# Kernel tuning notes

Hardware: AMD Instinct MI355X
Metric: run time of the kernel (lower is better)

Reference implementation:

```python
import jax, jax.numpy as jnp
import numpy as np

NUM_EMB = 512
LATENT = 20


def setup_inputs() -> dict:
    key = jax.random.key(0)
    ks = jax.random.split(key, 10)
    B = 262144
    c = jax.random.normal(ks[0], (B, 100), dtype=jnp.float32)
    W1 = jax.random.normal(ks[1], (100, 200), dtype=jnp.float32) * 0.1
    b1 = jnp.zeros((200,), dtype=jnp.float32)
    W2 = jax.random.normal(ks[2], (200, LATENT), dtype=jnp.float32) * 0.07
    b2 = jnp.zeros((LATENT,), dtype=jnp.float32)
    # codebook initialized uniform(-1/K, 1/K) as in torch
    codebook = jax.random.uniform(ks[3], (NUM_EMB, LATENT), dtype=jnp.float32,
                                  minval=-1.0 / NUM_EMB, maxval=1.0 / NUM_EMB)
    Wmu = jax.random.normal(ks[4], (LATENT, LATENT), dtype=jnp.float32) * 0.2
    bmu = jnp.zeros((LATENT,), dtype=jnp.float32)
    Wlv = jax.random.normal(ks[5], (LATENT, LATENT), dtype=jnp.float32) * 0.2
    blv = jnp.zeros((LATENT,), dtype=jnp.float32)
    return {"c": c, "W1": W1, "b1": b1, "W2": W2, "b2": b2,
            "codebook": codebook, "Wmu": Wmu, "bmu": bmu, "Wlv": Wlv, "blv": blv}


def reference(c, W1, b1, W2, b2, codebook, Wmu, bmu, Wlv, blv):
    # encoder: Linear -> ELU -> Linear
    h = jax.nn.elu(c @ W1 + b1)            # [B, 200]
    z_e = h @ W2 + b2                      # [B, 20]

    # vector quantization: pairwise squared distances to codebook
    d = (jnp.sum(z_e ** 2, axis=1, keepdims=True)
         + jnp.sum(codebook ** 2, axis=1)
         - 2.0 * z_e @ codebook.T)         # [B, K]
    idx = jnp.argmin(d, axis=1)            # [B]
    quantized = codebook[idx]              # [B, 20] gather

    commitment_loss = 0.25 * jnp.mean((jax.lax.stop_gradient(quantized) - z_e) ** 2)
    quantization_loss = jnp.mean((quantized - jax.lax.stop_gradient(z_e)) ** 2)
    z_q = z_e + jax.lax.stop_gradient(quantized - z_e)  # straight-through

    mu_c = z_e @ Wmu + bmu
    logvar_c = z_e @ Wlv + blv
    return (mu_c, logvar_c, z_q, z_e, quantization_loss, commitment_loss)
```

## Files before the change

### kernel.cpp

```cpp
#include <hip/hip_runtime.h>

typedef __bf16 bf16x8 __attribute__((ext_vector_type(8)));
typedef __bf16 bf16x4 __attribute__((ext_vector_type(4)));
typedef float  f32x4  __attribute__((ext_vector_type(4)));
typedef float  f32x2  __attribute__((ext_vector_type(2)));

constexpr int BN  = 262144;
constexpr int DIN = 100;
constexpr int DH  = 200;
constexpr int DZ  = 20;
constexpr int KCB = 512;

constexpr size_t WS_W1F  = 0;
constexpr size_t WS_W2F  = 53248;
constexpr size_t WS_CBF  = 69632;
constexpr size_t WS_WMUF = 102400;
constexpr size_t WS_WLVF = 104448;
constexpr size_t WS_B1P  = 106496;
constexpr size_t WS_B2P  = 107520;
constexpr size_t WS_BMUP = 107648;
constexpr size_t WS_BLVP = 107776;
constexpr size_t WS_PART = 107904;

constexpr int PN_W1 = 26624, PN_W2 = 8192, PN_CB = 16384, PN_WMU = 1024, PN_WLV = 1024;
constexpr int PN_TOT = PN_W1 + PN_W2 + PN_CB + PN_WMU + PN_WLV + 256 + 32 + 32 + 32;

__device__ __forceinline__ unsigned umin2(unsigned a, unsigned b) { return a < b ? a : b; }

__global__ __launch_bounds__(256) void prep_kernel(
    const float* __restrict__ W1, const float* __restrict__ b1,
    const float* __restrict__ W2, const float* __restrict__ b2,
    const float* __restrict__ cb,
    const float* __restrict__ Wmu, const float* __restrict__ bmu,
    const float* __restrict__ Wlv, const float* __restrict__ blv,
    unsigned char* __restrict__ ws)
{
    int e = blockIdx.x * 256 + threadIdx.x;
    if (e >= PN_TOT) return;
    __bf16* w1f  = (__bf16*)(ws + WS_W1F);
    __bf16* w2f  = (__bf16*)(ws + WS_W2F);
    __bf16* cbf  = (__bf16*)(ws + WS_CBF);
    __bf16* wmuf = (__bf16*)(ws + WS_WMUF);
    __bf16* wlvf = (__bf16*)(ws + WS_WLVF);
    float* b1p  = (float*)(ws + WS_B1P);
    float* b2p  = (float*)(ws + WS_B2P);
    float* bmup = (float*)(ws + WS_BMUP);
    float* blvp = (float*)(ws + WS_BLVP);

    if (e < PN_W1) {
        int j = e & 7, lane = (e >> 3) & 63, kk = (e >> 9) & 3, m = e >> 11;
        int n = m * 16 + (lane & 15);
        int k = kk * 32 + ((lane >> 4) << 3) + j;
        w1f[e] = (__bf16)((n < DH && k < DIN) ? W1[k * DH + n] : 0.f);
        return;
    }
    e -= PN_W1;
    if (e < PN_W2) {
        int j = e & 7, lane = (e >> 3) & 63, kk = (e >> 9) & 7, m2 = e >> 12;
        int n = m2 * 16 + (lane & 15);
        int k = kk * 32 + ((lane >> 4) << 3) + j;
        w2f[e] = (__bf16)((n < DZ && k < DH) ? W2[k * DZ + n] : 0.f);
        return;
    }
    e -= PN_W2;
    if (e < PN_CB) {
        int j = e & 7, lane = (e >> 3) & 63, ct = e >> 9;
        int code = ct * 16 + (lane & 15);
        int d = ((lane >> 4) << 3) + j;
        float v = 0.f;
        if (d < DZ) v = -2.f * cb[code * DZ + d];
        else if (d == DZ) {
            float s = 0.f;
            #pragma unroll
            for (int dd = 0; dd < DZ; ++dd) s = fmaf(cb[code * DZ + dd], cb[code * DZ + dd], s);
            v = s;
        }
        cbf[e] = (__bf16)v;
        return;
    }
    e -= PN_CB;
    if (e < PN_WMU) {
        int j = e & 7, lane = (e >> 3) & 63, m2 = e >> 9;
        int n = m2 * 16 + (lane & 15);
        int k = ((lane >> 4) << 3) + j;
        wmuf[e] = (__bf16)((n < DZ && k < DZ) ? Wmu[k * DZ + n] : 0.f);
        return;
    }
    e -= PN_WMU;
    if (e < PN_WLV) {
        int j = e & 7, lane = (e >> 3) & 63, m2 = e >> 9;
        int n = m2 * 16 + (lane & 15);
        int k = ((lane >> 4) << 3) + j;
        wlvf[e] = (__bf16)((n < DZ && k < DZ) ? Wlv[k * DZ + n] : 0.f);
        return;
    }
    e -= PN_WLV;
    if (e < 256) { b1p[e] = (e < DH) ? b1[e] : 0.f; return; }
    e -= 256;
    if (e < 32) { b2p[e] = (e < DZ) ? b2[e] : 0.f; return; }
    e -= 32;
    if (e < 32) { bmup[e] = (e < DZ) ? bmu[e] : 0.f; return; }
    e -= 32;
    blvp[e - 32] = (e - 32 < DZ) ? blv[e - 32] : 0.f;
}

__global__ __launch_bounds__(256) void fused_main(
    const float* __restrict__ c, const float* __restrict__ cb,
    const unsigned char* __restrict__ ws, float* __restrict__ out,
    float* __restrict__ partials)
{
    __shared__ __align__(16) unsigned char region[32768];

    const __bf16* w1f  = (const __bf16*)(ws + WS_W1F);
    const __bf16* w2f  = (const __bf16*)(ws + WS_W2F);
    const __bf16* cbf  = (const __bf16*)(ws + WS_CBF);
    const __bf16* wmuf = (const __bf16*)(ws + WS_WMUF);
    const __bf16* wlvf = (const __bf16*)(ws + WS_WLVF);
    const float* b1p  = (const float*)(ws + WS_B1P);
    const float* b2p  = (const float*)(ws + WS_B2P);
    const float* bmup = (const float*)(ws + WS_BMUP);
    const float* blvp = (const float*)(ws + WS_BLVP);

    const int tid = threadIdx.x;
    const int l   = tid & 63;
    const int wid = __builtin_amdgcn_readfirstlane(tid >> 6);
    const int g   = l >> 4;
    const int li  = l & 15;
    const int rowB = blockIdx.x * 128;

    {
        const float4* cbase = (const float4*)(c + (size_t)rowB * DIN);
        #pragma unroll
        for (int i = 0; i < 13; ++i) {
            int f4 = tid + i * 256;
            if (i < 12 || tid < 128) {
                float4 v = cbase[f4];
                int row = f4 / 25;
                int k4  = (f4 - row * 25) * 4;
                bf16x4 p;
                p[0] = (__bf16)v.x; p[1] = (__bf16)v.y;
                p[2] = (__bf16)v.z; p[3] = (__bf16)v.w;
                int byte = (k4 * 2) ^ ((row & 7) << 4);
                *(bf16x4*)(region + row * 256 + byte) = p;
            }
        }
        #pragma unroll
        for (int i = 0; i < 4; ++i) {
            int e = tid + i * 256;
            if (e < 896) {
                int row = e / 7, s = e - row * 7;
                int byte = (200 + s * 8) ^ ((row & 7) << 4);
                *(uint2*)(region + row * 256 + byte) = uint2{0u, 0u};
            }
        }
    }
    __syncthreads();

    bf16x8 cf0[4], cf1[4];
    #pragma unroll
    for (int nt = 0; nt < 2; ++nt) {
        const int row = wid * 32 + nt * 16 + li;
        const unsigned char* rb = region + row * 256;
        const int swz = (row & 7) << 4;
        #pragma unroll
        for (int kk = 0; kk < 4; ++kk) {
            bf16x8 a = *(const bf16x8*)(rb + ((kk * 64 + g * 16) ^ swz));
            if (nt == 0) cf0[kk] = a; else cf1[kk] = a;
        }
    }

    f32x4 zm0n0, zm0n1, zm1n0, zm1n1;
    {
        f32x4 bz0 = *(const f32x4*)(b2p + g * 4);
        f32x4 bz1 = *(const f32x4*)(b2p + 16 + g * 4);
        zm0n0 = bz0; zm0n1 = bz0; zm1n0 = bz1; zm1n1 = bz1;
    }

    unsigned char* hW = region + wid * 8192;
    const int swzH = (li & 7) << 4;

    #pragma unroll
    for (int hf = 0; hf < 2; ++hf) {
        #pragma unroll
        for (int mloc = 0; mloc < 8; ++mloc) {
            const int mg = hf * 8 + mloc;
            const int cbyte = (mloc * 32 + g * 8) ^ swzH;
            if (mg <= 12) {
                f32x4 acc0 = *(const f32x4*)(b1p + mg * 16 + g * 4);
                f32x4 acc1 = acc0;
                #pragma unroll
                for (int kk = 0; kk < 4; ++kk) {
                    bf16x8 aw = *(const bf16x8*)(w1f + ((mg * 4 + kk) * 512 + l * 8));
                    acc0 = __builtin_amdgcn_mfma_f32_16x16x32_bf16(aw, cf0[kk], acc0, 0, 0, 0);
                    acc1 = __builtin_amdgcn_mfma_f32_16x16x32_bf16(aw, cf1[kk], acc1, 0, 0, 0);
                }
                bf16x4 p0, p1;
                #pragma unroll
                for (int r = 0; r < 4; ++r) {
                    float h0 = acc0[r]; h0 = h0 > 0.f ? h0 : (__expf(h0) - 1.f);
                    float h1 = acc1[r]; h1 = h1 > 0.f ? h1 : (__expf(h1) - 1.f);
                    p0[r] = (__bf16)h0; p1[r] = (__bf16)h1;
                }
                *(bf16x4*)(hW + li * 256 + cbyte)        = p0;
                *(bf16x4*)(hW + (li + 16) * 256 + cbyte) = p1;
            } else {
                *(uint2*)(hW + li * 256 + cbyte)        = uint2{0u, 0u};
                *(uint2*)(hW + (li + 16) * 256 + cbyte) = uint2{0u, 0u};
            }
        }
        #pragma unroll
        for (int kk = 0; kk < 4; ++kk) {
            const int kk2 = hf * 4 + kk;
            const int rb = (kk * 64 + g * 16) ^ swzH;
            bf16x8 hb0 = *(const bf16x8*)(hW + li * 256 + rb);
            bf16x8 hb1 = *(const bf16x8*)(hW + (li + 16) * 256 + rb);
            bf16x8 w20 = *(const bf16x8*)(w2f + ((0 * 8 + kk2) * 512 + l * 8));
            bf16x8 w21 = *(const bf16x8*)(w2f + ((1 * 8 + kk2) * 512 + l * 8));
            zm0n0 = __builtin_amdgcn_mfma_f32_16x16x32_bf16(w20, hb0, zm0n0, 0, 0, 0);
            zm0n1 = __builtin_amdgcn_mfma_f32_16x16x32_bf16(w20, hb1, zm0n1, 0, 0, 0);
            zm1n0 = __builtin_amdgcn_mfma_f32_16x16x32_bf16(w21, hb0, zm1n0, 0, 0, 0);
            zm1n1 = __builtin_amdgcn_mfma_f32_16x16x32_bf16(w21, hb1, zm1n1, 0, 0, 0);
        }
    }

    unsigned char* zB = hW;
    const int swzZ = (li & 3) << 4;
    {
        bf16x4 q;
        #pragma unroll
        for (int r = 0; r < 4; ++r) q[r] = (__bf16)zm0n0[r];
        *(bf16x4*)(zB + li * 64 + ((g * 8) ^ swzZ)) = q;
        #pragma unroll
        for (int r = 0; r < 4; ++r) q[r] = (__bf16)zm0n1[r];
        *(bf16x4*)(zB + (li + 16) * 64 + ((g * 8) ^ swzZ)) = q;
        bf16x4 t0 = bf16x4{(__bf16)0.f, (__bf16)0.f, (__bf16)0.f, (__bf16)0.f};
        bf16x4 t1 = t0;
        if (g == 0) {
            #pragma unroll
            for (int r = 0; r < 4; ++r) { t0[r] = (__bf16)zm1n0[r]; t1[r] = (__bf16)zm1n1[r]; }
        } else if (g == 1) { t0[0] = (__bf16)1.0f; t1[0] = (__bf16)1.0f; }
        *(bf16x4*)(zB + li * 64 + ((32 + g * 8) ^ swzZ)) = t0;
        *(bf16x4*)(zB + (li + 16) * 64 + ((32 + g * 8) ^ swzZ)) = t1;
    }

    bf16x8 za0 = *(const bf16x8*)(zB + li * 64 + ((g * 16) ^ swzZ));
    bf16x8 za1 = *(const bf16x8*)(zB + (li + 16) * 64 + ((g * 16) ^ swzZ));
    __syncthreads();

    unsigned run0 = 0xFFFFFFFFu, run1 = 0xFFFFFFFFu;
    const f32x4 one4 = f32x4{1.f, 1.f, 1.f, 1.f};
    #pragma unroll 8
    for (int ct = 0; ct < 32; ++ct) {
        bf16x8 cf = *(const bf16x8*)(cbf + (ct * 512 + l * 8));
        f32x4 s0 = __builtin_amdgcn_mfma_f32_16x16x32_bf16(cf, za0, one4, 0, 0, 0);
        f32x4 s1 = __builtin_amdgcn_mfma_f32_16x16x32_bf16(cf, za1, one4, 0, 0, 0);
        const unsigned ib = (unsigned)(ct * 16 + g * 4);
        unsigned k0 = (__float_as_uint(s0[0]) & ~511u) | ib;
        unsigned k1 = (__float_as_uint(s0[1]) & ~511u) | (ib + 1);
        unsigned k2 = (__float_as_uint(s0[2]) & ~511u) | (ib + 2);
        unsigned k3 = (__float_as_uint(s0[3]) & ~511u) | (ib + 3);
        run0 = umin2(run0, umin2(umin2(k0, k1), umin2(k2, k3)));
        k0 = (__float_as_uint(s1[0]) & ~511u) | ib;
        k1 = (__float_as_uint(s1[1]) & ~511u) | (ib + 1);
        k2 = (__float_as_uint(s1[2]) & ~511u) | (ib + 2);
        k3 = (__float_as_uint(s1[3]) & ~511u) | (ib + 3);
        run1 = umin2(run1, umin2(umin2(k0, k1), umin2(k2, k3)));
    }
    run0 = umin2(run0, (unsigned)__shfl_xor((int)run0, 16, 64));
    run0 = umin2(run0, (unsigned)__shfl_xor((int)run0, 32, 64));
    run1 = umin2(run1, (unsigned)__shfl_xor((int)run1, 16, 64));
    run1 = umin2(run1, (unsigned)__shfl_xor((int)run1, 32, 64));
    const int idx0 = (int)(run0 & 511u);
    const int idx1 = (int)(run1 & 511u);

    f32x4 mu00, mu01, mu10, mu11, lv00, lv01, lv10, lv11;
    {
        f32x4 bm0 = *(const f32x4*)(bmup + g * 4);
        f32x4 bm1 = *(const f32x4*)(bmup + 16 + g * 4);
        f32x4 bv0 = *(const f32x4*)(blvp + g * 4);
        f32x4 bv1 = *(const f32x4*)(blvp + 16 + g * 4);
        bf16x8 wm0 = *(const bf16x8*)(wmuf + (0 * 512 + l * 8));
        bf16x8 wm1 = *(const bf16x8*)(wmuf + (1 * 512 + l * 8));
        bf16x8 wl0 = *(const bf16x8*)(wlvf + (0 * 512 + l * 8));
        bf16x8 wl1 = *(const bf16x8*)(wlvf + (1 * 512 + l * 8));
        mu00 = __builtin_amdgcn_mfma_f32_16x16x32_bf16(wm0, za0, bm0, 0, 0, 0);
        mu01 = __builtin_amdgcn_mfma_f32_16x16x32_bf16(wm0, za1, bm0, 0, 0, 0);
        mu10 = __builtin_amdgcn_mfma_f32_16x16x32_bf16(wm1, za0, bm1, 0, 0, 0);
        mu11 = __builtin_amdgcn_mfma_f32_16x16x32_bf16(wm1, za1, bm1, 0, 0, 0);
        lv00 = __builtin_amdgcn_mfma_f32_16x16x32_bf16(wl0, za0, bv0, 0, 0, 0);
        lv01 = __builtin_amdgcn_mfma_f32_16x16x32_bf16(wl0, za1, bv0, 0, 0, 0);
        lv10 = __builtin_amdgcn_mfma_f32_16x16x32_bf16(wl1, za0, bv1, 0, 0, 0);
        lv11 = __builtin_amdgcn_mfma_f32_16x16x32_bf16(wl1, za1, bv1, 0, 0, 0);
    }

    float lsum = 0.f;
    float4 q00 = *(const float4*)(cb + idx0 * DZ + g * 4);
    float4 q10 = *(const float4*)(cb + idx1 * DZ + g * 4);
    {
        float d;
        d = q00.x - zm0n0[0]; lsum = fmaf(d, d, lsum);
        d = q00.y - zm0n0[1]; lsum = fmaf(d, d, lsum);
        d = q00.z - zm0n0[2]; lsum = fmaf(d, d, lsum);
        d = q00.w - zm0n0[3]; lsum = fmaf(d, d, lsum);
        d = q10.x - zm0n1[0]; lsum = fmaf(d, d, lsum);
        d = q10.y - zm0n1[1]; lsum = fmaf(d, d, lsum);
        d = q10.z - zm0n1[2]; lsum = fmaf(d, d, lsum);
        d = q10.w - zm0n1[3]; lsum = fmaf(d, d, lsum);
    }
    float4 qe0 = make_float4(0.f, 0.f, 0.f, 0.f), qe1 = qe0;
    if (g == 0) {
        qe0 = *(const float4*)(cb + idx0 * DZ + 16);
        qe1 = *(const float4*)(cb + idx1 * DZ + 16);
        float d;
        d = qe0.x - zm1n0[0]; lsum = fmaf(d, d, lsum);
        d = qe0.y - zm1n0[1]; lsum = fmaf(d, d, lsum);
        d = qe0.z - zm1n0[2]; lsum = fmaf(d, d, lsum);
        d = qe0.w - zm1n0[3]; lsum = fmaf(d, d, lsum);
        d = qe1.x - zm1n1[0]; lsum = fmaf(d, d, lsum);
        d = qe1.y - zm1n1[1]; lsum = fmaf(d, d, lsum);
        d = qe1.z - zm1n1[2]; lsum = fmaf(d, d, lsum);
        d = qe1.w - zm1n1[3]; lsum = fmaf(d, d, lsum);
    }
    #pragma unroll
    for (int off = 32; off > 0; off >>= 1) lsum += __shfl_down(lsum, off, 64);
    if (l == 0) partials[blockIdx.x * 4 + wid] = lsum;

    const size_t SEC = (size_t)BN * DZ;
    const size_t obase = (size_t)rowB * DZ;
    float* o_mu = out + obase;
    float* o_lv = out + SEC + obase;
    float* o_zq = out + 2 * SEC + obase;
    float* o_ze = out + 3 * SEC + obase;

    float* sA = (float*)region;
    float* sB = (float*)region + 2560;
    const int r0 = wid * 32 + li, r1 = r0 + 16;

    *(float4*)(sA + r0 * DZ + g * 4) = *(float4*)&mu00;
    *(float4*)(sA + r1 * DZ + g * 4) = *(float4*)&mu01;
    *(float4*)(sB + r0 * DZ + g * 4) = *(float4*)&lv00;
    *(float4*)(sB + r1 * DZ + g * 4) = *(float4*)&lv01;
    if (g == 0) {
        *(float4*)(sA + r0 * DZ + 16) = *(float4*)&mu10;
        *(float4*)(sA + r1 * DZ + 16) = *(float4*)&mu11;
        *(float4*)(sB + r0 * DZ + 16) = *(float4*)&lv10;
        *(float4*)(sB + r1 * DZ + 16) = *(float4*)&lv11;
    }
    __syncthreads();
    #pragma unroll
    for (int i = 0; i < 5; ++i) {
        int w = tid * 2 + i * 512;
        __builtin_nontemporal_store(*(const f32x2*)(sA + w), (f32x2*)(o_mu + w));
        __builtin_nontemporal_store(*(const f32x2*)(sB + w), (f32x2*)(o_lv + w));
    }
    __syncthreads();

    *(float4*)(sA + r0 * DZ + g * 4) = q00;
    *(float4*)(sA + r1 * DZ + g * 4) = q10;
    *(float4*)(sB + r0 * DZ + g * 4) = *(float4*)&zm0n0;
    *(float4*)(sB + r1 * DZ + g * 4) = *(float4*)&zm0n1;
    if (g == 0) {
        *(float4*)(sA + r0 * DZ + 16) = qe0;
        *(float4*)(sA + r1 * DZ + 16) = qe1;
        *(float4*)(sB + r0 * DZ + 16) = *(float4*)&zm1n0;
        *(float4*)(sB + r1 * DZ + 16) = *(float4*)&zm1n1;
    }
    __syncthreads();
    #pragma unroll
    for (int i = 0; i < 5; ++i) {
        int w = tid * 2 + i * 512;
        __builtin_nontemporal_store(*(const f32x2*)(sA + w), (f32x2*)(o_zq + w));
        __builtin_nontemporal_store(*(const f32x2*)(sB + w), (f32x2*)(o_ze + w));
    }
}

__global__ __launch_bounds__(256) void loss_reduce(const float* __restrict__ partials,
                                                   float* __restrict__ out_scalars) {
    int t = threadIdx.x;
    float s = 0.f;
    #pragma unroll
    for (int i = 0; i < 32; ++i) s += partials[t + 256 * i];
    #pragma unroll
    for (int off = 32; off > 0; off >>= 1) s += __shfl_down(s, off, 64);
    __shared__ float wsum[4];
    if ((t & 63) == 0) wsum[t >> 6] = s;
    __syncthreads();
    if (t == 0) {
        float total = (wsum[0] + wsum[1]) + (wsum[2] + wsum[3]);
        float ql = total / (float)((size_t)BN * DZ);
        out_scalars[0] = ql;
        out_scalars[1] = 0.25f * ql;
    }
}

extern "C" void kernel_launch(void* const* d_in, const int* in_sizes, int n_in,
                              void* d_out, int out_size, void* d_ws, size_t ws_size,
                              hipStream_t stream) {
    const float* c   = (const float*)d_in[0];
    const float* W1  = (const float*)d_in[1];
    const float* b1  = (const float*)d_in[2];
    const float* W2  = (const float*)d_in[3];
    const float* b2  = (const float*)d_in[4];
    const float* cb  = (const float*)d_in[5];
    const float* Wmu = (const float*)d_in[6];
    const float* bmu = (const float*)d_in[7];
    const float* Wlv = (const float*)d_in[8];
    const float* blv = (const float*)d_in[9];
    float* out = (float*)d_out;
    unsigned char* ws = (unsigned char*)d_ws;
    float* partials = (float*)(ws + WS_PART);

    prep_kernel<<<(PN_TOT + 255) / 256, 256, 0, stream>>>(
        W1, b1, W2, b2, cb, Wmu, bmu, Wlv, blv, ws);
    fused_main<<<BN / 128, 256, 0, stream>>>(c, cb, ws, out, partials);
    loss_reduce<<<1, 256, 0, stream>>>(partials, out + 4 * (size_t)BN * DZ);
}
```

Before: 82.95 us.

## Shrink LDS footprint with 224-byte input rows and per-wave hidden chunking

The input tile now uses an unswizzled 224-byte row stride in shared memory. Zero padding is written once per row, and the last K chunk is zeroed in registers instead of being read from LDS. The hidden-layer staging is split into four 64-wide chunks, each feeding the second GEMM right away, so each wave needs 7 KB instead of 8 KB and total LDS falls from 32 KB to 28 KB, aiming at higher occupancy and fewer zero-fill stores. Dropping the swizzle on the input rows may add LDS bank conflicts, and the extra chunk boundaries add more interleaving of the two GEMMs.

Measured after the change: 117.0 us. 41.0% more time.

```diff
diff --git a/kernel.cpp b/kernel.cpp
--- a/kernel.cpp
+++ b/kernel.cpp
@@ -109,7 +109,7 @@
     const unsigned char* __restrict__ ws, float* __restrict__ out,
     float* __restrict__ partials)
 {
-    __shared__ __align__(16) unsigned char region[32768];
+    __shared__ __align__(16) unsigned char region[28672];
 
     const __bf16* w1f  = (const __bf16*)(ws + WS_W1F);
     const __bf16* w2f  = (const __bf16*)(ws + WS_W2F);
@@ -140,19 +140,10 @@
                 bf16x4 p;
                 p[0] = (__bf16)v.x; p[1] = (__bf16)v.y;
                 p[2] = (__bf16)v.z; p[3] = (__bf16)v.w;
-                int byte = (k4 * 2) ^ ((row & 7) << 4);
-                *(bf16x4*)(region + row * 256 + byte) = p;
+                *(bf16x4*)(region + row * 224 + k4 * 2) = p;
             }
         }
-        #pragma unroll
-        for (int i = 0; i < 4; ++i) {
-            int e = tid + i * 256;
-            if (e < 896) {
-                int row = e / 7, s = e - row * 7;
-                int byte = (200 + s * 8) ^ ((row & 7) << 4);
-                *(uint2*)(region + row * 256 + byte) = uint2{0u, 0u};
-            }
-        }
+        if (tid < 128) *(uint2*)(region + tid * 224 + 200) = uint2{0u, 0u};
     }
     __syncthreads();
 
@@ -160,13 +151,16 @@
     #pragma unroll
     for (int nt = 0; nt < 2; ++nt) {
         const int row = wid * 32 + nt * 16 + li;
-        const unsigned char* rb = region + row * 256;
-        const int swz = (row & 7) << 4;
-        #pragma unroll
-        for (int kk = 0; kk < 4; ++kk) {
-            bf16x8 a = *(const bf16x8*)(rb + ((kk * 64 + g * 16) ^ swz));
-            if (nt == 0) cf0[kk] = a; else cf1[kk] = a;
-        }
+        const unsigned char* rb = region + row * 224;
+        bf16x8 a0 = *(const bf16x8*)(rb + 0 * 64 + g * 16);
+        bf16x8 a1 = *(const bf16x8*)(rb + 1 * 64 + g * 16);
+        bf16x8 a2 = *(const bf16x8*)(rb + 2 * 64 + g * 16);
+        bf16x8 a3;
+        #pragma unroll
+        for (int j = 0; j < 8; ++j) a3[j] = (__bf16)0.f;
+        if (g == 0) a3 = *(const bf16x8*)(rb + 192);
+        if (nt == 0) { cf0[0] = a0; cf0[1] = a1; cf0[2] = a2; cf0[3] = a3; }
+        else         { cf1[0] = a0; cf1[1] = a1; cf1[2] = a2; cf1[3] = a3; }
     }
 
     f32x4 zm0n0, zm0n1, zm1n0, zm1n1;
@@ -176,44 +170,41 @@
         zm0n0 = bz0; zm0n1 = bz0; zm1n0 = bz1; zm1n1 = bz1;
     }
 
-    unsigned char* hW = region + wid * 8192;
+    unsigned char* hB = region + wid * 7168;
     const int swzH = (li & 7) << 4;
 
     #pragma unroll
-    for (int hf = 0; hf < 2; ++hf) {
-        #pragma unroll
-        for (int mloc = 0; mloc < 8; ++mloc) {
-            const int mg = hf * 8 + mloc;
-            const int cbyte = (mloc * 32 + g * 8) ^ swzH;
-            if (mg <= 12) {
-                f32x4 acc0 = *(const f32x4*)(b1p + mg * 16 + g * 4);
-                f32x4 acc1 = acc0;
-                #pragma unroll
-                for (int kk = 0; kk < 4; ++kk) {
-                    bf16x8 aw = *(const bf16x8*)(w1f + ((mg * 4 + kk) * 512 + l * 8));
-                    acc0 = __builtin_amdgcn_mfma_f32_16x16x32_bf16(aw, cf0[kk], acc0, 0, 0, 0);
-                    acc1 = __builtin_amdgcn_mfma_f32_16x16x32_bf16(aw, cf1[kk], acc1, 0, 0, 0);
-                }
-                bf16x4 p0, p1;
-                #pragma unroll
-                for (int r = 0; r < 4; ++r) {
-                    float h0 = acc0[r]; h0 = h0 > 0.f ? h0 : (__expf(h0) - 1.f);
-                    float h1 = acc1[r]; h1 = h1 > 0.f ? h1 : (__expf(h1) - 1.f);
-                    p0[r] = (__bf16)h0; p1[r] = (__bf16)h1;
-                }
-                *(bf16x4*)(hW + li * 256 + cbyte)        = p0;
-                *(bf16x4*)(hW + (li + 16) * 256 + cbyte) = p1;
-            } else {
-                *(uint2*)(hW + li * 256 + cbyte)        = uint2{0u, 0u};
-                *(uint2*)(hW + (li + 16) * 256 + cbyte) = uint2{0u, 0u};
+    for (int w = 0; w < 4; ++w) {
+        #pragma unroll
+        for (int tl = 0; tl < 4; ++tl) {
+            if (w == 3 && tl > 0) continue;
+            const int mg = w * 4 + tl;
+            f32x4 acc0 = *(const f32x4*)(b1p + mg * 16 + g * 4);
+            f32x4 acc1 = acc0;
+            #pragma unroll
+            for (int kk = 0; kk < 4; ++kk) {
+                bf16x8 aw = *(const bf16x8*)(w1f + ((mg * 4 + kk) * 512 + l * 8));
+                acc0 = __builtin_amdgcn_mfma_f32_16x16x32_bf16(aw, cf0[kk], acc0, 0, 0, 0);
+                acc1 = __builtin_amdgcn_mfma_f32_16x16x32_bf16(aw, cf1[kk], acc1, 0, 0, 0);
             }
+            bf16x4 p0, p1;
+            #pragma unroll
+            for (int r = 0; r < 4; ++r) {
+                float h0 = acc0[r]; h0 = h0 > 0.f ? h0 : (__expf(h0) - 1.f);
+                float h1 = acc1[r]; h1 = h1 > 0.f ? h1 : (__expf(h1) - 1.f);
+                p0[r] = (__bf16)h0; p1[r] = (__bf16)h1;
+            }
+            const int hbyte = (tl * 32 + g * 8) ^ swzH;
+            *(bf16x4*)(hB + li * 128 + hbyte)        = p0;
+            *(bf16x4*)(hB + (li + 16) * 128 + hbyte) = p1;
         }
         #pragma unroll
-        for (int kk = 0; kk < 4; ++kk) {
-            const int kk2 = hf * 4 + kk;
-            const int rb = (kk * 64 + g * 16) ^ swzH;
-            bf16x8 hb0 = *(const bf16x8*)(hW + li * 256 + rb);
-            bf16x8 hb1 = *(const bf16x8*)(hW + (li + 16) * 256 + rb);
+        for (int kl = 0; kl < 2; ++kl) {
+            if (w == 3 && kl == 1) continue;
+            const int kk2 = w * 2 + kl;
+            const int rb2 = (kl * 64 + g * 16) ^ swzH;
+            bf16x8 hb0 = *(const bf16x8*)(hB + li * 128 + rb2);
+            bf16x8 hb1 = *(const bf16x8*)(hB + (li + 16) * 128 + rb2);
             bf16x8 w20 = *(const bf16x8*)(w2f + ((0 * 8 + kk2) * 512 + l * 8));
             bf16x8 w21 = *(const bf16x8*)(w2f + ((1 * 8 + kk2) * 512 + l * 8));
             zm0n0 = __builtin_amdgcn_mfma_f32_16x16x32_bf16(w20, hb0, zm0n0, 0, 0, 0);
@@ -223,7 +214,7 @@
         }
     }
 
-    unsigned char* zB = hW;
+    unsigned char* zB = hB;
     const int swzZ = (li & 3) << 4;
     {
         bf16x4 q;
@@ -233,7 +224,9 @@
         #pragma unroll
         for (int r = 0; r < 4; ++r) q[r] = (__bf16)zm0n1[r];
         *(bf16x4*)(zB + (li + 16) * 64 + ((g * 8) ^ swzZ)) = q;
-        bf16x4 t0 = bf16x4{(__bf16)0.f, (__bf16)0.f, (__bf16)0.f, (__bf16)0.f};
+        bf16x4 t0;
+        #pragma unroll
+        for (int r = 0; r < 4; ++r) t0[r] = (__bf16)0.f;
         bf16x4 t1 = t0;
         if (g == 0) {
             #pragma unroll
@@ -248,23 +241,24 @@
     __syncthreads();
 
     unsigned run0 = 0xFFFFFFFFu, run1 = 0xFFFFFFFFu;
-    const f32x4 one4 = f32x4{1.f, 1.f, 1.f, 1.f};
+    f32x4 one4;
+    one4[0] = 1.f; one4[1] = 1.f; one4[2] = 1.f; one4[3] = 1.f;
     #pragma unroll 8
     for (int ct = 0; ct < 32; ++ct) {
         bf16x8 cf = *(const bf16x8*)(cbf + (ct * 512 + l * 8));
         f32x4 s0 = __builtin_amdgcn_mfma_f32_16x16x32_bf16(cf, za0, one4, 0, 0, 0);
         f32x4 s1 = __builtin_amdgcn_mfma_f32_16x16x32_bf16(cf, za1, one4, 0, 0, 0);
         const unsigned ib = (unsigned)(ct * 16 + g * 4);
-        unsigned k0 = (__float_as_uint(s0[0]) & ~511u) | ib;
-        unsigned k1 = (__float_as_uint(s0[1]) & ~511u) | (ib + 1);
-        unsigned k2 = (__float_as_uint(s0[2]) & ~511u) | (ib + 2);
-        unsigned k3 = (__float_as_uint(s0[3]) & ~511u) | (ib + 3);
-        run0 = umin2(run0, umin2(umin2(k0, k1), umin2(k2, k3)));
-        k0 = (__float_as_uint(s1[0]) & ~511u) | ib;
-        k1 = (__float_as_uint(s1[1]) & ~511u) | (ib + 1);
-        k2 = (__float_as_uint(s1[2]) & ~511u) | (ib + 2);
-        k3 = (__float_as_uint(s1[3]) & ~511u) | (ib + 3);
-        run1 = umin2(run1, umin2(umin2(k0, k1), umin2(k2, k3)));
+        unsigned k0 = (__float_as_uint(s0[0]) & ~511u) | ((ib + 0) & 511u);
+        unsigned k1 = (__float_as_uint(s0[1]) & ~511u) | ((ib + 1) & 511u);
+        unsigned k2 = (__float_as_uint(s0[2]) & ~511u) | ((ib + 2) & 511u);
+        unsigned k3 = (__float_as_uint(s0[3]) & ~511u) | ((ib + 3) & 511u);
+        run0 = umin2(umin2(k0, k1), umin2(umin2(k2, k3), run0));
+        k0 = (__float_as_uint(s1[0]) & ~511u) | ((ib + 0) & 511u);
+        k1 = (__float_as_uint(s1[1]) & ~511u) | ((ib + 1) & 511u);
+        k2 = (__float_as_uint(s1[2]) & ~511u) | ((ib + 2) & 511u);
+        k3 = (__float_as_uint(s1[3]) & ~511u) | ((ib + 3) & 511u);
+        run1 = umin2(umin2(k0, k1), umin2(umin2(k2, k3), run1));
     }
     run0 = umin2(run0, (unsigned)__shfl_xor((int)run0, 16, 64));
     run0 = umin2(run0, (unsigned)__shfl_xor((int)run0, 32, 64));
```
